# Optimization experiments

Hardware: AMD Instinct MI355X
Metric: run time of the kernel (lower is better)

## Reference

```python
import jax, jax.numpy as jnp
import numpy as np

INPUT_SIZE = 512
HIDDEN_SIZE = 256
B, S = 8, 2048


def setup_inputs() -> dict:
    key = jax.random.key(0)
    ks = jax.random.split(key, 9)
    d = INPUT_SIZE
    q = jax.random.normal(ks[0], (B, S, 2 * HIDDEN_SIZE), dtype=jnp.float32)
    k = jax.random.normal(ks[1], (B, S, d), dtype=jnp.float32)
    v = jax.random.normal(ks[2], (B, S, d), dtype=jnp.float32)
    # Params: module uses nn.init.normal_ (std=1); keep normal but scale for stability.
    Wq = jax.random.normal(ks[3], (2 * HIDDEN_SIZE, d), dtype=jnp.float32) * 0.02
    bq = jax.random.normal(ks[4], (d,), dtype=jnp.float32) * 0.02
    Wk = jax.random.normal(ks[5], (d, d), dtype=jnp.float32) * 0.02
    bk = jax.random.normal(ks[6], (d,), dtype=jnp.float32) * 0.02
    Wv = jax.random.normal(ks[7], (d, d), dtype=jnp.float32) * 0.02
    bv = jax.random.normal(ks[8], (d,), dtype=jnp.float32) * 0.02
    return {"q": q, "k": k, "v": v, "Wq": Wq, "bq": bq, "Wk": Wk, "bk": bk, "Wv": Wv, "bv": bv}


def reference(q, k, v, Wq, bq, Wk, bk, Wv, bv):
    d = Wq.shape[-1]
    qp = jnp.einsum('bsh,hd->bsd', q, Wq) + bq  # [B,S,d]
    kp = jnp.einsum('bse,ed->bsd', k, Wk) + bk
    vp = jnp.einsum('bse,ed->bsd', v, Wv) + bv
    scale = 1.0 / jnp.sqrt(jnp.float32(d))
    scores = jnp.einsum('bqd,bkd->bqk', qp, kp) * scale  # [B,S,S]
    attn = jax.nn.softmax(scores, axis=-1)
    return jnp.einsum('bqk,bkd->bqd', attn, vp)
```

## Files before the change

### kernel.cpp

```cpp
#include <hip/hip_runtime.h>
#include <hip/hip_bf16.h>
#include <stdint.h>


typedef __attribute__((ext_vector_type(8))) short short8;
typedef __attribute__((ext_vector_type(4))) float floatx4;

__device__ __forceinline__ unsigned short f2bf(float f) {
    union { float f; uint32_t u; } v; v.f = f;
    uint32_t u = v.u;
    return (unsigned short)((u + 0x7FFF + ((u >> 16) & 1)) >> 16);
}

#define ASYNC16(g, l)                                                          \
    __builtin_amdgcn_global_load_lds(                                          \
        (const __attribute__((address_space(1))) unsigned int*)(g),            \
        (__attribute__((address_space(3))) unsigned int*)(l), 16, 0, 0)

__global__ void wt_kernel(const float* __restrict__ Wq, const float* __restrict__ Wk,
                          const float* __restrict__ Wv, unsigned short* __restrict__ WT) {
    __shared__ float t[64][65];
    const int z = blockIdx.z;
    const float* W = (z == 0) ? Wq : ((z == 1) ? Wk : Wv);
    const int n0 = blockIdx.x * 64, k0 = blockIdx.y * 64;
    const int tx = threadIdx.x & 63, ty = threadIdx.x >> 6;
#pragma unroll
    for (int i = ty; i < 64; i += 4) t[i][tx] = W[(size_t)(k0 + i) * 512 + n0 + tx];
    __syncthreads();
#pragma unroll
    for (int i = ty; i < 64; i += 4)
        WT[(size_t)z * 262144 + (size_t)(n0 + i) * 512 + k0 + tx] = f2bf(t[tx][i]);
}

__global__ __launch_bounds__(256, 2) void proj_kernel(
    const float* __restrict__ q, const float* __restrict__ k, const float* __restrict__ v,
    const float* __restrict__ bq, const float* __restrict__ bk, const float* __restrict__ bv,
    const unsigned short* __restrict__ WT,
    unsigned short* __restrict__ qp, unsigned short* __restrict__ kp,
    unsigned short* __restrict__ vpT)
{
    __shared__ __align__(16) unsigned short At[2][64][32];
    __shared__ __align__(16) unsigned short Bt[2][512][32];

    const int z = blockIdx.z;
    const int lane = threadIdx.x & 63;
    const int wave = threadIdx.x >> 6;
    const int col = lane & 15;
    const int quad = lane >> 4;

    const float* A = (z == 0) ? q : ((z == 1) ? k : v);
    const float* bias = (z == 0) ? bq : ((z == 1) ? bk : bv);
    const unsigned short* W = WT + (size_t)z * 262144;

    const int m0 = blockIdx.x * 64;
    const int n0w = wave * 128;

    floatx4 acc[4][8];
#pragma unroll
    for (int mf = 0; mf < 4; ++mf)
#pragma unroll
        for (int nf = 0; nf < 8; ++nf) acc[mf][nf] = floatx4{0.f, 0.f, 0.f, 0.f};

    auto stageB = [&](int nb, int kc) {
#pragma unroll
        for (int jj = 0; jj < 8; ++jj) {
            const int j = wave * 8 + jj;
            const int row = j * 16 + (lane >> 2);
            const unsigned short* g =
                W + (size_t)row * 512 + kc * 32 + (((lane & 3) ^ (row & 3)) << 3);
            ASYNC16(g, &Bt[nb][j * 16][0]);
        }
    };
    auto stageA = [&](int nb, int kc) {
        const int row = wave * 16 + (lane >> 2);
        const float* ap = A + (size_t)(m0 + row) * 512 + kc * 32 + (lane & 3) * 8;
        float4 f0 = *(const float4*)ap;
        float4 f1 = *(const float4*)(ap + 4);
        short8 t;
        t[0] = f2bf(f0.x); t[1] = f2bf(f0.y); t[2] = f2bf(f0.z); t[3] = f2bf(f0.w);
        t[4] = f2bf(f1.x); t[5] = f2bf(f1.y); t[6] = f2bf(f1.z); t[7] = f2bf(f1.w);
        *(short8*)&At[nb][row][((lane & 3) ^ (row & 3)) << 3] = t;
    };

    stageB(0, 0);
    stageA(0, 0);
    for (int kc = 0; kc < 16; ++kc) {
        const int cur = kc & 1;
        __syncthreads();
        if (kc < 15) { stageB(cur ^ 1, kc + 1); stageA(cur ^ 1, kc + 1); }

        short8 a[4], bfr[8];
#pragma unroll
        for (int mf = 0; mf < 4; ++mf)
            a[mf] = *(const short8*)&At[cur][mf * 16 + col][(quad ^ (col & 3)) << 3];
#pragma unroll
        for (int nf = 0; nf < 8; ++nf)
            bfr[nf] = *(const short8*)&Bt[cur][n0w + nf * 16 + col][(quad ^ (col & 3)) << 3];
#pragma unroll
        for (int mf = 0; mf < 4; ++mf)
#pragma unroll
            for (int nf = 0; nf < 8; ++nf)
                acc[mf][nf] = __builtin_amdgcn_mfma_f32_16x16x32_bf16(a[mf], bfr[nf], acc[mf][nf], 0, 0, 0);
    }

    const float scale = (z == 0) ? 0.04419417382415922f : 1.0f;
#pragma unroll
    for (int mf = 0; mf < 4; ++mf) {
#pragma unroll
        for (int nf = 0; nf < 8; ++nf) {
            const int n = n0w + nf * 16 + col;
            const float bn2 = bias[n];
            floatx4 c = acc[mf][nf];
            if (z < 2) {
                unsigned short* outp = (z == 0) ? qp : kp;
#pragma unroll
                for (int r = 0; r < 4; ++r) {
                    int row = m0 + mf * 16 + quad * 4 + r;
                    outp[(size_t)row * 512 + n] = f2bf((c[r] + bn2) * scale);
                }
            } else {
                int row = m0 + mf * 16 + quad * 4;
                int bb = row >> 11;
                int s = row & 2047;
                ushort4 pk;
                pk.x = f2bf(c[0] + bn2); pk.y = f2bf(c[1] + bn2);
                pk.z = f2bf(c[2] + bn2); pk.w = f2bf(c[3] + bn2);
                *(ushort4*)(vpT + (((size_t)bb * 64 + (s >> 5)) * 512 + n) * 32 + (s & 31)) = pk;
            }
        }
    }
}

__global__ __launch_bounds__(256, 1) void attn_kernel(
    const unsigned short* __restrict__ qp, const unsigned short* __restrict__ kp,
    const unsigned short* __restrict__ vpT, float* __restrict__ out)
{
    __shared__ __align__(16) unsigned short Kt[2][32][512];
    __shared__ __align__(16) unsigned short Vt[2][512][32];
    __shared__ __align__(16) unsigned short Pbuf[4][16][40];

    const int lane = threadIdx.x & 63;
    const int wave = threadIdx.x >> 6;
    const int col = lane & 15;
    const int quad = lane >> 4;
    const int b = blockIdx.x & 7;
    const int qt = blockIdx.x >> 3;
    const int q0 = qt * 64 + wave * 16;
    const size_t rowbase = (size_t)b * 2048 + q0;

    const unsigned short* kpb = kp + (size_t)b * 2048 * 512;
    const unsigned short* vpb = vpT + ((size_t)b << 20);

    short8 aq[16];
#pragma unroll
    for (int ks = 0; ks < 16; ++ks)
        aq[ks] = *(const short8*)(qp + (rowbase + col) * 512 + ks * 32 + quad * 8);

    floatx4 o[32];
#pragma unroll
    for (int i = 0; i < 32; ++i) o[i] = floatx4{0.f, 0.f, 0.f, 0.f};
    float plsum[4] = {0.f, 0.f, 0.f, 0.f};

    auto stage = [&](int nb, int keyblk) {
#pragma unroll
        for (int j = 0; j < 8; ++j) {
            const int r = wave * 8 + j;
            const unsigned short* g =
                kpb + ((size_t)(keyblk * 32 + r) << 9) + ((lane ^ (r & 7)) << 3);
            ASYNC16(g, &Kt[nb][r][0]);
        }
        const unsigned short* vtile = vpb + ((size_t)keyblk << 14);
#pragma unroll
        for (int jj = 0; jj < 8; ++jj) {
            const int j2 = wave * 8 + jj;
            const int d = j2 * 16 + (lane >> 2);
            const unsigned short* g =
                vtile + ((size_t)d << 5) + (((lane & 3) ^ (d & 3)) << 3);
            ASYNC16(g, &Vt[nb][j2 * 16][0]);
        }
    };

    stage(0, 0);
    for (int kb = 0; kb < 64; ++kb) {
        const int cur = kb & 1;
        __syncthreads();
        if (kb < 63) stage(cur ^ 1, kb + 1);

        floatx4 s0 = floatx4{0.f, 0.f, 0.f, 0.f};
        floatx4 s1 = floatx4{0.f, 0.f, 0.f, 0.f};
#pragma unroll
        for (int ks = 0; ks < 16; ++ks) {
            const int c = (ks << 2) + quad;
            short8 b0 = *(const short8*)&Kt[cur][col][(c ^ (col & 7)) << 3];
            short8 b1 = *(const short8*)&Kt[cur][16 + col][(c ^ (col & 7)) << 3];
            s0 = __builtin_amdgcn_mfma_f32_16x16x32_bf16(aq[ks], b0, s0, 0, 0, 0);
            s1 = __builtin_amdgcn_mfma_f32_16x16x32_bf16(aq[ks], b1, s1, 0, 0, 0);
        }

#pragma unroll
        for (int r = 0; r < 4; ++r) {
            const float p0 = __expf(s0[r]);
            const float p1 = __expf(s1[r]);
            plsum[r] += p0 + p1;
            Pbuf[wave][quad * 4 + r][col]      = f2bf(p0);
            Pbuf[wave][quad * 4 + r][16 + col] = f2bf(p1);
        }
        const short8 aP = *(const short8*)&Pbuf[wave][col][quad * 8];

#pragma unroll
        for (int nf = 0; nf < 32; ++nf) {
            const int d = nf * 16 + col;
            short8 bvf = *(const short8*)&Vt[cur][d][(quad ^ (d & 3)) << 3];
            o[nf] = __builtin_amdgcn_mfma_f32_16x16x32_bf16(aP, bvf, o[nf], 0, 0, 0);
        }
    }

    float l[4];
#pragma unroll
    for (int r = 0; r < 4; ++r) {
        float acc_s = plsum[r];
#pragma unroll
        for (int off = 1; off <= 8; off <<= 1)
            acc_s += __shfl_xor(acc_s, off, 64);
        l[r] = acc_s;
    }
#pragma unroll
    for (int nf = 0; nf < 32; ++nf) {
#pragma unroll
        for (int r = 0; r < 4; ++r) {
            out[(rowbase + quad * 4 + r) * 512 + nf * 16 + col] = o[nf][r] / l[r];
        }
    }
}

extern "C" void kernel_launch(void* const* d_in, const int* in_sizes, int n_in,
                              void* d_out, int out_size, void* d_ws, size_t ws_size,
                              hipStream_t stream) {
    const float* q  = (const float*)d_in[0];
    const float* k  = (const float*)d_in[1];
    const float* v  = (const float*)d_in[2];
    const float* Wq = (const float*)d_in[3];
    const float* bq = (const float*)d_in[4];
    const float* Wk = (const float*)d_in[5];
    const float* bk = (const float*)d_in[6];
    const float* Wv = (const float*)d_in[7];
    const float* bv = (const float*)d_in[8];
    float* out = (float*)d_out;

    unsigned short* WT  = (unsigned short*)d_ws;
    unsigned short* qp  = WT + (size_t)3 * 262144;
    unsigned short* kp  = qp + (size_t)16384 * 512;
    unsigned short* vpT = kp + (size_t)16384 * 512;

    wt_kernel<<<dim3(8, 8, 3), 256, 0, stream>>>(Wq, Wk, Wv, WT);
    proj_kernel<<<dim3(256, 1, 3), 256, 0, stream>>>(q, k, v, bq, bk, bv, WT, qp, kp, vpT);
    attn_kernel<<<256, 256, 0, stream>>>(qp, kp, vpT, out);
}
```

Measured before the change: 369.7 us.

## Drop LDS staging in attention, give each wave 32 query rows, prefetch A in projection

Result: slower. 796.8 us (+115.5%).

```diff
diff --git a/kernel.cpp b/kernel.cpp
--- a/kernel.cpp
+++ b/kernel.cpp
@@ -54,6 +54,7 @@
 
     const int m0 = blockIdx.x * 64;
     const int n0w = wave * 128;
+    const int arow = wave * 16 + (lane >> 2);
 
     floatx4 acc[4][8];
 #pragma unroll
@@ -71,23 +72,32 @@
             ASYNC16(g, &Bt[nb][j * 16][0]);
         }
     };
-    auto stageA = [&](int nb, int kc) {
-        const int row = wave * 16 + (lane >> 2);
-        const float* ap = A + (size_t)(m0 + row) * 512 + kc * 32 + (lane & 3) * 8;
-        float4 f0 = *(const float4*)ap;
-        float4 f1 = *(const float4*)(ap + 4);
+    auto loadA = [&](float4& f0, float4& f1, int kc) {
+        const float* ap = A + (size_t)(m0 + arow) * 512 + kc * 32 + (lane & 3) * 8;
+        f0 = *(const float4*)ap;
+        f1 = *(const float4*)(ap + 4);
+    };
+    auto writeA = [&](int nb, const float4& f0, const float4& f1) {
         short8 t;
         t[0] = f2bf(f0.x); t[1] = f2bf(f0.y); t[2] = f2bf(f0.z); t[3] = f2bf(f0.w);
         t[4] = f2bf(f1.x); t[5] = f2bf(f1.y); t[6] = f2bf(f1.z); t[7] = f2bf(f1.w);
-        *(short8*)&At[nb][row][((lane & 3) ^ (row & 3)) << 3] = t;
+        *(short8*)&At[nb][arow][((lane & 3) ^ (arow & 3)) << 3] = t;
     };
 
+    float4 ra0, ra1;
     stageB(0, 0);
-    stageA(0, 0);
+    loadA(ra0, ra1, 0);
+    writeA(0, ra0, ra1);
+    loadA(ra0, ra1, 1);
+
     for (int kc = 0; kc < 16; ++kc) {
         const int cur = kc & 1;
         __syncthreads();
-        if (kc < 15) { stageB(cur ^ 1, kc + 1); stageA(cur ^ 1, kc + 1); }
+        if (kc < 15) {
+            stageB(cur ^ 1, kc + 1);
+            writeA(cur ^ 1, ra0, ra1);
+        }
+        if (kc < 14) loadA(ra0, ra1, kc + 2);
 
         short8 a[4], bfr[8];
 #pragma unroll
@@ -131,106 +141,95 @@
     }
 }
 
-__global__ __launch_bounds__(256, 1) void attn_kernel(
+__global__ __launch_bounds__(128, 1) void attn_kernel(
     const unsigned short* __restrict__ qp, const unsigned short* __restrict__ kp,
     const unsigned short* __restrict__ vpT, float* __restrict__ out)
 {
-    __shared__ __align__(16) unsigned short Kt[2][32][512];
-    __shared__ __align__(16) unsigned short Vt[2][512][32];
-    __shared__ __align__(16) unsigned short Pbuf[4][16][40];
+    __shared__ __align__(16) unsigned short Pbuf[2][32][40];
 
     const int lane = threadIdx.x & 63;
-    const int wave = threadIdx.x >> 6;
+    const int w = threadIdx.x >> 6;
     const int col = lane & 15;
     const int quad = lane >> 4;
     const int b = blockIdx.x & 7;
     const int qt = blockIdx.x >> 3;
-    const int q0 = qt * 64 + wave * 16;
+    const int q0 = qt * 64 + w * 32;
     const size_t rowbase = (size_t)b * 2048 + q0;
 
     const unsigned short* kpb = kp + (size_t)b * 2048 * 512;
     const unsigned short* vpb = vpT + ((size_t)b << 20);
 
-    short8 aq[16];
-#pragma unroll
-    for (int ks = 0; ks < 16; ++ks)
-        aq[ks] = *(const short8*)(qp + (rowbase + col) * 512 + ks * 32 + quad * 8);
-
-    floatx4 o[32];
-#pragma unroll
-    for (int i = 0; i < 32; ++i) o[i] = floatx4{0.f, 0.f, 0.f, 0.f};
-    float plsum[4] = {0.f, 0.f, 0.f, 0.f};
-
-    auto stage = [&](int nb, int keyblk) {
-#pragma unroll
-        for (int j = 0; j < 8; ++j) {
-            const int r = wave * 8 + j;
-            const unsigned short* g =
-                kpb + ((size_t)(keyblk * 32 + r) << 9) + ((lane ^ (r & 7)) << 3);
-            ASYNC16(g, &Kt[nb][r][0]);
-        }
-        const unsigned short* vtile = vpb + ((size_t)keyblk << 14);
-#pragma unroll
-        for (int jj = 0; jj < 8; ++jj) {
-            const int j2 = wave * 8 + jj;
-            const int d = j2 * 16 + (lane >> 2);
-            const unsigned short* g =
-                vtile + ((size_t)d << 5) + (((lane & 3) ^ (d & 3)) << 3);
-            ASYNC16(g, &Vt[nb][j2 * 16][0]);
-        }
-    };
-
-    stage(0, 0);
+    short8 aq[2][16];
+#pragma unroll
+    for (int mt = 0; mt < 2; ++mt)
+#pragma unroll
+        for (int ks = 0; ks < 16; ++ks)
+            aq[mt][ks] = *(const short8*)(qp + (rowbase + mt * 16 + col) * 512 + ks * 32 + quad * 8);
+
+    floatx4 o[2][32];
+#pragma unroll
+    for (int mt = 0; mt < 2; ++mt)
+#pragma unroll
+        for (int dt = 0; dt < 32; ++dt) o[mt][dt] = floatx4{0.f, 0.f, 0.f, 0.f};
+    float plsum[2][4] = {{0.f, 0.f, 0.f, 0.f}, {0.f, 0.f, 0.f, 0.f}};
+
     for (int kb = 0; kb < 64; ++kb) {
-        const int cur = kb & 1;
-        __syncthreads();
-        if (kb < 63) stage(cur ^ 1, kb + 1);
-
-        floatx4 s0 = floatx4{0.f, 0.f, 0.f, 0.f};
-        floatx4 s1 = floatx4{0.f, 0.f, 0.f, 0.f};
+        const int key0 = kb * 32;
+        const unsigned short* vtile = vpb + ((size_t)kb << 14);
+
+        floatx4 s[2][2];
+        s[0][0] = floatx4{0.f, 0.f, 0.f, 0.f}; s[0][1] = floatx4{0.f, 0.f, 0.f, 0.f};
+        s[1][0] = floatx4{0.f, 0.f, 0.f, 0.f}; s[1][1] = floatx4{0.f, 0.f, 0.f, 0.f};
 #pragma unroll
         for (int ks = 0; ks < 16; ++ks) {
-            const int c = (ks << 2) + quad;
-            short8 b0 = *(const short8*)&Kt[cur][col][(c ^ (col & 7)) << 3];
-            short8 b1 = *(const short8*)&Kt[cur][16 + col][(c ^ (col & 7)) << 3];
-            s0 = __builtin_amdgcn_mfma_f32_16x16x32_bf16(aq[ks], b0, s0, 0, 0, 0);
-            s1 = __builtin_amdgcn_mfma_f32_16x16x32_bf16(aq[ks], b1, s1, 0, 0, 0);
-        }
-
+            short8 b0 = *(const short8*)(kpb + (size_t)(key0 + col) * 512 + ks * 32 + quad * 8);
+            short8 b1 = *(const short8*)(kpb + (size_t)(key0 + 16 + col) * 512 + ks * 32 + quad * 8);
+            s[0][0] = __builtin_amdgcn_mfma_f32_16x16x32_bf16(aq[0][ks], b0, s[0][0], 0, 0, 0);
+            s[1][0] = __builtin_amdgcn_mfma_f32_16x16x32_bf16(aq[1][ks], b0, s[1][0], 0, 0, 0);
+            s[0][1] = __builtin_amdgcn_mfma_f32_16x16x32_bf16(aq[0][ks], b1, s[0][1], 0, 0, 0);
+            s[1][1] = __builtin_amdgcn_mfma_f32_16x16x32_bf16(aq[1][ks], b1, s[1][1], 0, 0, 0);
+        }
+
+#pragma unroll
+        for (int mt = 0; mt < 2; ++mt)
+#pragma unroll
+            for (int r = 0; r < 4; ++r) {
+                const float p0 = __expf(s[mt][0][r]);
+                const float p1 = __expf(s[mt][1][r]);
+                plsum[mt][r] += p0 + p1;
+                Pbuf[w][mt * 16 + quad * 4 + r][col]      = f2bf(p0);
+                Pbuf[w][mt * 16 + quad * 4 + r][16 + col] = f2bf(p1);
+            }
+        const short8 aP0 = *(const short8*)&Pbuf[w][col][quad * 8];
+        const short8 aP1 = *(const short8*)&Pbuf[w][16 + col][quad * 8];
+
+#pragma unroll
+        for (int dt = 0; dt < 32; ++dt) {
+            short8 bv = *(const short8*)(vtile + (size_t)(dt * 16 + col) * 32 + quad * 8);
+            o[0][dt] = __builtin_amdgcn_mfma_f32_16x16x32_bf16(aP0, bv, o[0][dt], 0, 0, 0);
+            o[1][dt] = __builtin_amdgcn_mfma_f32_16x16x32_bf16(aP1, bv, o[1][dt], 0, 0, 0);
+        }
+    }
+
+    float l[2][4];
+#pragma unroll
+    for (int mt = 0; mt < 2; ++mt)
 #pragma unroll
         for (int r = 0; r < 4; ++r) {
-            const float p0 = __expf(s0[r]);
-            const float p1 = __expf(s1[r]);
-            plsum[r] += p0 + p1;
-            Pbuf[wave][quad * 4 + r][col]      = f2bf(p0);
-            Pbuf[wave][quad * 4 + r][16 + col] = f2bf(p1);
-        }
-        const short8 aP = *(const short8*)&Pbuf[wave][col][quad * 8];
-
-#pragma unroll
-        for (int nf = 0; nf < 32; ++nf) {
-            const int d = nf * 16 + col;
-            short8 bvf = *(const short8*)&Vt[cur][d][(quad ^ (d & 3)) << 3];
-            o[nf] = __builtin_amdgcn_mfma_f32_16x16x32_bf16(aP, bvf, o[nf], 0, 0, 0);
-        }
-    }
-
-    float l[4];
-#pragma unroll
-    for (int r = 0; r < 4; ++r) {
-        float acc_s = plsum[r];
-#pragma unroll
-        for (int off = 1; off <= 8; off <<= 1)
-            acc_s += __shfl_xor(acc_s, off, 64);
-        l[r] = acc_s;
-    }
-#pragma unroll
-    for (int nf = 0; nf < 32; ++nf) {
-#pragma unroll
-        for (int r = 0; r < 4; ++r) {
-            out[(rowbase + quad * 4 + r) * 512 + nf * 16 + col] = o[nf][r] / l[r];
-        }
-    }
+            float acc_s = plsum[mt][r];
+#pragma unroll
+            for (int off = 1; off <= 8; off <<= 1)
+                acc_s += __shfl_xor(acc_s, off, 64);
+            l[mt][r] = acc_s;
+        }
+#pragma unroll
+    for (int mt = 0; mt < 2; ++mt)
+#pragma unroll
+        for (int dt = 0; dt < 32; ++dt)
+#pragma unroll
+            for (int r = 0; r < 4; ++r)
+                out[(rowbase + mt * 16 + quad * 4 + r) * 512 + dt * 16 + col] =
+                    o[mt][dt][r] / l[mt][r];
 }
 
 extern "C" void kernel_launch(void* const* d_in, const int* in_sizes, int n_in,
@@ -254,5 +253,5 @@
 
     wt_kernel<<<dim3(8, 8, 3), 256, 0, stream>>>(Wq, Wk, Wv, WT);
     proj_kernel<<<dim3(256, 1, 3), 256, 0, stream>>>(q, k, v, bq, bk, bv, WT, qp, kp, vpT);
-    attn_kernel<<<256, 256, 0, stream>>>(qp, kp, vpT, out);
-}
+    attn_kernel<<<256, 128, 0, stream>>>(qp, kp, vpT, out);
+}
```
